# Optimization experiments

Measured on AMD Instinct MI355X. Metric: run time of the kernel, lower is better.

The kernel has to match this reference:

```python
import jax, jax.numpy as jnp
import numpy as np

BN_EPS = 1e-5


def setup_inputs() -> dict:
    key = jax.random.key(0)
    ks = jax.random.split(key, 10)
    B, C, L = 16, 512, 1024
    scale = 1.0 / np.sqrt(C)
    inp = {
        "x": jax.random.normal(ks[0], (B, C, L), dtype=jnp.float32),
        "gamma": jnp.ones((C,), jnp.float32),
        "beta": jnp.zeros((C,), jnp.float32),
        "Wq": jax.random.normal(ks[1], (C, C), jnp.float32) * scale,
        "bq": jnp.zeros((C,), jnp.float32),
        "Wk": jax.random.normal(ks[2], (C, C), jnp.float32) * scale,
        "bk": jnp.zeros((C,), jnp.float32),
        "Wv": jax.random.normal(ks[3], (C, C), jnp.float32) * scale,
        "bv": jnp.zeros((C,), jnp.float32),
        "Wp": jax.random.normal(ks[4], (C, C), jnp.float32) * scale,
        "bp": jnp.zeros((C,), jnp.float32),
    }
    return inp


def _pointwise(W, b, h):
    # Conv1d with kernel_size=1 == per-position linear: [C_out,C_in] x [B,C_in,L]
    return jnp.einsum("oc,bcl->bol", W, h) + b[None, :, None]


def reference(x, gamma, beta, Wq, bq, Wk, bk, Wv, bv, Wp, bp):
    B, C, L = x.shape
    # BatchNorm1d (training-mode batch statistics over batch & length dims)
    mean = jnp.mean(x, axis=(0, 2), keepdims=True)
    var = jnp.var(x, axis=(0, 2), keepdims=True)
    hn = (x - mean) * jax.lax.rsqrt(var + BN_EPS)
    hn = hn * gamma[None, :, None] + beta[None, :, None]

    q = _pointwise(Wq, bq, hn)  # [B,C,L]
    k = _pointwise(Wk, bk, hn)
    v = _pointwise(Wv, bv, hn)

    # attn[b,i,j] = sum_c q[b,c,i] k[b,c,j] / sqrt(C); i=query pos, j=key pos
    attn = jnp.einsum("bci,bcj->bij", q, k) * (C ** -0.5)
    attn = jax.nn.softmax(attn, axis=-1)

    # out[b,c,i] = sum_j attn[b,i,j] v[b,c,j]
    h_ = jnp.einsum("bij,bcj->bci", attn, v)
    h_ = _pointwise(Wp, bp, h_)
    return x + h_
```

## Files before the change

kernel.cpp:

```cpp
#include <hip/hip_runtime.h>
#include <hip/hip_bf16.h>


#define BB 16
#define CC 512
#define LL 1024

typedef __bf16 bf16x8 __attribute__((ext_vector_type(8)));
typedef float  f32x4  __attribute__((ext_vector_type(4)));

__device__ inline unsigned short bf16_bits(float f) {
  __hip_bfloat16 h = __float2bfloat16(f);
  return __builtin_bit_cast(unsigned short, h);
}
__device__ inline float bits_lo(unsigned int u) {
  return __builtin_bit_cast(float, u << 16);
}
__device__ inline float bits_hi(unsigned int u) {
  return __builtin_bit_cast(float, u & 0xffff0000u);
}

__global__ __launch_bounds__(256) void bn_stats(
    const float* __restrict__ x, const float* __restrict__ gamma,
    const float* __restrict__ beta, float* __restrict__ scl,
    float* __restrict__ sft) {
  int c = blockIdx.x;
  int t = threadIdx.x;
  float s = 0.f, s2 = 0.f;
  for (int b = 0; b < BB; ++b) {
    float4 v = ((const float4*)(x + ((size_t)(b * CC + c)) * LL))[t];
    s  += v.x + v.y + v.z + v.w;
    s2 += v.x * v.x + v.y * v.y + v.z * v.z + v.w * v.w;
  }
  for (int m = 32; m; m >>= 1) { s += __shfl_xor(s, m, 64); s2 += __shfl_xor(s2, m, 64); }
  __shared__ float rs[4], rs2[4];
  int wave = t >> 6, lane = t & 63;
  if (lane == 0) { rs[wave] = s; rs2[wave] = s2; }
  __syncthreads();
  if (t == 0) {
    float S  = rs[0] + rs[1] + rs[2] + rs[3];
    float S2 = rs2[0] + rs2[1] + rs2[2] + rs2[3];
    float mean = S * (1.f / 16384.f);
    float var  = S2 * (1.f / 16384.f) - mean * mean;
    float sc = gamma[c] * rsqrtf(var + 1e-5f);
    scl[c] = sc;
    sft[c] = beta[c] - mean * sc;
  }
}

__global__ __launch_bounds__(256) void cast4(
    const float* __restrict__ Wq, const float* __restrict__ Wk,
    const float* __restrict__ Wv, const float* __restrict__ Wp,
    __hip_bfloat16* __restrict__ Wqk, __hip_bfloat16* __restrict__ Wvb,
    __hip_bfloat16* __restrict__ Wpb) {
  int m = blockIdx.y;
  const float* src = m == 0 ? Wq : m == 1 ? Wk : m == 2 ? Wv : Wp;
  __hip_bfloat16* dst = m == 0 ? Wqk : m == 1 ? Wqk + 262144 : m == 2 ? Wvb : Wpb;
  int i = blockIdx.x * 256 + threadIdx.x;
  float4 v = ((const float4*)src)[i];
  ushort4 o;
  o.x = bf16_bits(v.x); o.y = bf16_bits(v.y);
  o.z = bf16_bits(v.z); o.w = bf16_bits(v.w);
  ((ushort4*)dst)[i] = o;
}

__global__ __launch_bounds__(256) void norm_t(
    const float* __restrict__ x, const float* __restrict__ scl,
    const float* __restrict__ sft, __hip_bfloat16* __restrict__ hnT) {
  __shared__ float tile[32][33];
  int l0 = blockIdx.x * 32, c0 = blockIdx.y * 32, b = blockIdx.z;
  int t = threadIdx.x;
#pragma unroll
  for (int i = 0; i < 4; ++i) {
    int idx = t + i * 256;
    int cc = idx >> 5, ll = idx & 31;
    tile[cc][ll] = x[((size_t)(b * CC + c0 + cc)) * LL + l0 + ll];
  }
  __syncthreads();
#pragma unroll
  for (int i = 0; i < 2; ++i) {
    int idx = t + i * 256;
    int ll = idx >> 4, cc = (idx & 15) * 2;
    float v0 = tile[cc][ll] * scl[c0 + cc] + sft[c0 + cc];
    float v1 = tile[cc + 1][ll] * scl[c0 + cc + 1] + sft[c0 + cc + 1];
    ushort2 o; o.x = bf16_bits(v0); o.y = bf16_bits(v1);
    *(ushort2*)(hnT + ((size_t)(b * LL + l0 + ll)) * CC + c0 + cc) = o;
  }
}

__global__ __launch_bounds__(256) void softmax_bf16(__hip_bfloat16* __restrict__ S) {
  int wave = threadIdx.x >> 6, lane = threadIdx.x & 63;
  size_t row = (size_t)blockIdx.x * 4 + wave;
  uint4* p = (uint4*)(S + row * 1024);
  uint4 r0 = p[lane * 2], r1 = p[lane * 2 + 1];
  float f[16];
  unsigned int w[8] = {r0.x, r0.y, r0.z, r0.w, r1.x, r1.y, r1.z, r1.w};
#pragma unroll
  for (int i = 0; i < 8; ++i) { f[2 * i] = bits_lo(w[i]); f[2 * i + 1] = bits_hi(w[i]); }
  float mx = f[0];
#pragma unroll
  for (int i = 1; i < 16; ++i) mx = fmaxf(mx, f[i]);
  for (int m = 32; m; m >>= 1) mx = fmaxf(mx, __shfl_xor(mx, m, 64));
  float s = 0.f;
#pragma unroll
  for (int i = 0; i < 16; ++i) { f[i] = __expf(f[i] - mx); s += f[i]; }
  for (int m = 32; m; m >>= 1) s += __shfl_xor(s, m, 64);
  float inv = 1.f / s;
  unsigned int ow[8];
#pragma unroll
  for (int i = 0; i < 8; ++i) {
    unsigned int lo = bf16_bits(f[2 * i] * inv);
    unsigned int hi = bf16_bits(f[2 * i + 1] * inv);
    ow[i] = lo | (hi << 16);
  }
  uint4 o0 = {ow[0], ow[1], ow[2], ow[3]}, o1 = {ow[4], ow[5], ow[6], ow[7]};
  p[lane * 2] = o0; p[lane * 2 + 1] = o1;
}

__device__ inline void glds(const __hip_bfloat16* g, __hip_bfloat16* l) {
  __builtin_amdgcn_global_load_lds(
      (__attribute__((address_space(1))) void*)(void*)g,
      (__attribute__((address_space(3))) void*)l, 16, 0, 0);
}

__device__ __forceinline__ void gemm_core(
    const __hip_bfloat16* __restrict__ A, int lda,
    const __hip_bfloat16* __restrict__ B, int ldb, int K,
    __hip_bfloat16* sm, f32x4 (&acc)[4][4]) {
  const int tid = threadIdx.x;
  const int wave = tid >> 6, lane = tid & 63;
  const int wm = (wave >> 1) * 64, wn = (wave & 1) * 64;
  const int row0 = tid >> 2;
  const int ke0 = (((tid & 3) ^ ((tid >> 3) & 3)) * 8);
  const int fr = lane & 15;
  const int q = lane >> 4;
  const int colA = ((q ^ ((fr >> 1) & 3)) * 8);
  const int dofs = wave * 512;

  const __hip_bfloat16* ga0 = A + (size_t)row0 * lda + ke0;
  const __hip_bfloat16* ga1 = ga0 + (size_t)64 * lda;
  const __hip_bfloat16* gb0 = B + (size_t)row0 * ldb + ke0;
  const __hip_bfloat16* gb1 = gb0 + (size_t)64 * ldb;

  __hip_bfloat16* rb = sm;
  __hip_bfloat16* nb = sm + 8192;
  __hip_bfloat16* wb = sm + 16384;

  const int niters = K >> 5;
  {
    glds(ga0, rb + dofs);          glds(ga1, rb + 2048 + dofs);
    glds(gb0, rb + 4096 + dofs);   glds(gb1, rb + 6144 + dofs);
    glds(ga0 + 32, nb + dofs);        glds(ga1 + 32, nb + 2048 + dofs);
    glds(gb0 + 32, nb + 4096 + dofs); glds(gb1 + 32, nb + 6144 + dofs);
  }
  for (int k = 0; k < niters; ++k) {
    if (k + 1 < niters) __builtin_amdgcn_s_waitcnt(0x0F74);
    else                __builtin_amdgcn_s_waitcnt(0x0F70);
    __builtin_amdgcn_s_barrier();
    if (k + 2 < niters) {
      int ko = (k + 2) * 32;
      glds(ga0 + ko, wb + dofs);          glds(ga1 + ko, wb + 2048 + dofs);
      glds(gb0 + ko, wb + 4096 + dofs);   glds(gb1 + ko, wb + 6144 + dofs);
    }
    bf16x8 af[4], bfr[4];
#pragma unroll
    for (int i = 0; i < 4; ++i) {
      af[i]  = *(const bf16x8*)(rb + (wm + i * 16 + fr) * 32 + colA);
      bfr[i] = *(const bf16x8*)(rb + 4096 + (wn + i * 16 + fr) * 32 + colA);
    }
#pragma unroll
    for (int i = 0; i < 4; ++i)
#pragma unroll
      for (int j = 0; j < 4; ++j)
        acc[i][j] = __builtin_amdgcn_mfma_f32_16x16x32_bf16(af[i], bfr[j], acc[i][j], 0, 0, 0);
    __hip_bfloat16* t = rb; rb = nb; nb = wb; wb = t;
  }
}

__global__ __launch_bounds__(256, 3) void gemm_qk(
    const __hip_bfloat16* __restrict__ Wb, const __hip_bfloat16* __restrict__ hnT,
    __hip_bfloat16* __restrict__ qT, __hip_bfloat16* __restrict__ kT,
    const float* __restrict__ bq, const float* __restrict__ bk) {
  __shared__ __align__(16) __hip_bfloat16 sm[3 * 8192];
  const int bat = blockIdx.z;
  const int m0 = blockIdx.y * 128, n0 = blockIdx.x * 128;
  f32x4 acc[4][4] = {};
  gemm_core(Wb + (size_t)m0 * 512, 512,
            hnT + (size_t)bat * LL * CC + (size_t)n0 * 512, 512, 512, sm, acc);
  const int lane = threadIdx.x & 63, wave = threadIdx.x >> 6;
  const int wm = (wave >> 1) * 64, wn = (wave & 1) * 64;
  const int crow = (lane >> 4) * 4, ccol = lane & 15;
  const int id = m0 >> 9;
  const int mloc0 = m0 & 511;
  const float* bias = id == 0 ? bq : bk;
  __hip_bfloat16* D = (id == 0 ? qT : kT) + (size_t)bat * LL * CC;
#pragma unroll
  for (int i = 0; i < 4; ++i) {
    int mg = mloc0 + wm + i * 16 + crow;
    float bv4[4];
#pragma unroll
    for (int r = 0; r < 4; ++r) bv4[r] = bias[mg + r];
#pragma unroll
    for (int j = 0; j < 4; ++j) {
      int ng = n0 + wn + j * 16 + ccol;
      ushort4 o;
      o.x = bf16_bits(acc[i][j][0] + bv4[0]);
      o.y = bf16_bits(acc[i][j][1] + bv4[1]);
      o.z = bf16_bits(acc[i][j][2] + bv4[2]);
      o.w = bf16_bits(acc[i][j][3] + bv4[3]);
      *(ushort4*)(D + (size_t)ng * 512 + mg) = o;
    }
  }
}

template <bool BIAS>
__global__ __launch_bounds__(256, 3) void gemm_bf16t(
    const __hip_bfloat16* __restrict__ A, int lda, size_t strideA,
    const __hip_bfloat16* __restrict__ B, int ldb, size_t strideB,
    __hip_bfloat16* __restrict__ D, int ldd, size_t strideD,
    const float* __restrict__ bias, float scale, int K) {
  __shared__ __align__(16) __hip_bfloat16 sm[3 * 8192];
  const int bat = blockIdx.z;
  const int m0 = blockIdx.y * 128, n0 = blockIdx.x * 128;
  f32x4 acc[4][4] = {};
  gemm_core(A + (size_t)bat * strideA + (size_t)m0 * lda, lda,
            B + (size_t)bat * strideB + (size_t)n0 * ldb, ldb, K, sm, acc);
  const int lane = threadIdx.x & 63, wave = threadIdx.x >> 6;
  const int wm = (wave >> 1) * 64, wn = (wave & 1) * 64;
  const int crow = (lane >> 4) * 4, ccol = lane & 15;
  __hip_bfloat16* Db = D + (size_t)bat * strideD;
#pragma unroll
  for (int j = 0; j < 4; ++j) {
    int ng = n0 + wn + j * 16 + ccol;
    float bn = BIAS ? bias[ng] : 0.f;
#pragma unroll
    for (int i = 0; i < 4; ++i) {
      int mg = m0 + wm + i * 16 + crow;
      ushort4 o;
      o.x = bf16_bits(acc[i][j][0] * scale + bn);
      o.y = bf16_bits(acc[i][j][1] * scale + bn);
      o.z = bf16_bits(acc[i][j][2] * scale + bn);
      o.w = bf16_bits(acc[i][j][3] * scale + bn);
      *(ushort4*)(Db + (size_t)ng * ldd + mg) = o;
    }
  }
}

__global__ __launch_bounds__(256, 3) void gemm_f32t(
    const __hip_bfloat16* __restrict__ A, int lda, size_t strideA,
    const __hip_bfloat16* __restrict__ B, int ldb,
    float* __restrict__ D, int ldd, size_t strideD,
    const float* __restrict__ bias, const float* __restrict__ resid, int K) {
  __shared__ __align__(16) __hip_bfloat16 sm[3 * 8192];
  const int bat = blockIdx.z;
  const int m0 = blockIdx.y * 128, n0 = blockIdx.x * 128;
  f32x4 acc[4][4] = {};
  gemm_core(A + (size_t)bat * strideA + (size_t)m0 * lda, lda,
            B + (size_t)n0 * ldb, ldb, K, sm, acc);
  const int lane = threadIdx.x & 63, wave = threadIdx.x >> 6;
  const int wm = (wave >> 1) * 64, wn = (wave & 1) * 64;
  const int crow = (lane >> 4) * 4, ccol = lane & 15;
  float* Db = D + (size_t)bat * strideD;
  const float* Rb = resid + (size_t)bat * strideD;
#pragma unroll
  for (int j = 0; j < 4; ++j) {
    int ng = n0 + wn + j * 16 + ccol;
    float bn = bias[ng];
#pragma unroll
    for (int i = 0; i < 4; ++i) {
      int mg = m0 + wm + i * 16 + crow;
      float4 r = *(const float4*)(Rb + (size_t)ng * ldd + mg);
      float4 o;
      o.x = acc[i][j][0] + bn + r.x;
      o.y = acc[i][j][1] + bn + r.y;
      o.z = acc[i][j][2] + bn + r.z;
      o.w = acc[i][j][3] + bn + r.w;
      *(float4*)(Db + (size_t)ng * ldd + mg) = o;
    }
  }
}

extern "C" void kernel_launch(void* const* d_in, const int* in_sizes, int n_in,
                              void* d_out, int out_size, void* d_ws, size_t ws_size,
                              hipStream_t stream) {
  const float* x     = (const float*)d_in[0];
  const float* gamma = (const float*)d_in[1];
  const float* beta  = (const float*)d_in[2];
  const float* Wq    = (const float*)d_in[3];
  const float* bq    = (const float*)d_in[4];
  const float* Wk    = (const float*)d_in[5];
  const float* bk    = (const float*)d_in[6];
  const float* Wv    = (const float*)d_in[7];
  const float* bv    = (const float*)d_in[8];
  const float* Wp    = (const float*)d_in[9];
  const float* bp    = (const float*)d_in[10];
  float* out = (float*)d_out;

  char* ws = (char*)d_ws;
  float* scl = (float*)ws;
  float* sft = scl + 512;
  __hip_bfloat16* Wqkb = (__hip_bfloat16*)(ws + 4096);
  __hip_bfloat16* Wvb  = Wqkb + 524288;
  __hip_bfloat16* Wpb  = Wvb + 262144;
  __hip_bfloat16* hnT  = Wpb + 262144;
  __hip_bfloat16* qT   = hnT + 8388608;
  __hip_bfloat16* kT   = qT + 8388608;
  __hip_bfloat16* vN   = kT + 8388608;
  __hip_bfloat16* Sb   = vN + 8388608;
  __hip_bfloat16* HT   = hnT;

  const size_t sLC = (size_t)LL * CC;
  const size_t sCL = (size_t)CC * LL;
  const size_t sLLb = (size_t)LL * LL;

  bn_stats<<<512, 256, 0, stream>>>(x, gamma, beta, scl, sft);
  cast4<<<dim3(256, 4), 256, 0, stream>>>(Wq, Wk, Wv, Wp, Wqkb, Wvb, Wpb);
  norm_t<<<dim3(32, 16, 16), 256, 0, stream>>>(x, scl, sft, hnT);

  gemm_qk<<<dim3(8, 8, 16), 256, 0, stream>>>(Wqkb, hnT, qT, kT, bq, bk);
  gemm_bf16t<true><<<dim3(4, 8, 16), 256, 0, stream>>>(
      hnT, 512, sLC, Wvb, 512, 0, vN, 1024, sCL, bv, 1.f, 512);
  gemm_bf16t<false><<<dim3(8, 8, 16), 256, 0, stream>>>(
      kT, 512, sLC, qT, 512, sLC, Sb, 1024, sLLb, nullptr,
      0.04419417382415922f, 512);
  softmax_bf16<<<4096, 256, 0, stream>>>(Sb);
  gemm_bf16t<false><<<dim3(8, 4, 16), 256, 0, stream>>>(
      vN, 1024, sCL, Sb, 1024, sLLb, HT, 512, sLC, nullptr, 1.f, 1024);
  gemm_f32t<<<dim3(4, 8, 16), 256, 0, stream>>>(
      HT, 512, sLC, Wpb, 512, out, 1024, sCL, bp, x, 512);
}
```

Before: 254.5 us.

## Fold Q/K projections into precomputed Wk^T·Wq bilinear form and simplify GEMM core

Attention scores are rewritten as hn^T (Wk^T Wq) hn plus a key-dependent bias term bq·Wk·hn. Terms that are constant along the softmax row are dropped, since softmax ignores them. A small 512x512 GEMM builds the combined matrix, a GEMV builds the per-key bias, and one fused launch produces both V and the transformed T1. This removes a full Q/K projection pass and its stored activations. Separately, the shared GEMM core drops its three-stage async LDS pipeline for a single-buffer loop with two barriers per K step, which risks exposing load latency in every GEMM. The combined matrix is also rounded to bf16, which adds precision risk.

```diff
diff --git a/kernel.cpp b/kernel.cpp
--- a/kernel.cpp
+++ b/kernel.cpp
@@ -5,6 +5,7 @@
 #define BB 16
 #define CC 512
 #define LL 1024
+#define SCALE 0.04419417382415922f
 
 typedef __bf16 bf16x8 __attribute__((ext_vector_type(8)));
 typedef float  f32x4  __attribute__((ext_vector_type(4)));
@@ -48,20 +49,52 @@
   }
 }
 
-__global__ __launch_bounds__(256) void cast4(
+__global__ __launch_bounds__(256) void cast_t(
     const float* __restrict__ Wq, const float* __restrict__ Wk,
     const float* __restrict__ Wv, const float* __restrict__ Wp,
-    __hip_bfloat16* __restrict__ Wqk, __hip_bfloat16* __restrict__ Wvb,
-    __hip_bfloat16* __restrict__ Wpb) {
+    const float* __restrict__ bq,
+    __hip_bfloat16* __restrict__ WqT, __hip_bfloat16* __restrict__ WkT,
+    __hip_bfloat16* __restrict__ Avt1, __hip_bfloat16* __restrict__ Wpb,
+    float* __restrict__ g2) {
   int m = blockIdx.y;
-  const float* src = m == 0 ? Wq : m == 1 ? Wk : m == 2 ? Wv : Wp;
-  __hip_bfloat16* dst = m == 0 ? Wqk : m == 1 ? Wqk + 262144 : m == 2 ? Wvb : Wpb;
-  int i = blockIdx.x * 256 + threadIdx.x;
-  float4 v = ((const float4*)src)[i];
-  ushort4 o;
-  o.x = bf16_bits(v.x); o.y = bf16_bits(v.y);
-  o.z = bf16_bits(v.z); o.w = bf16_bits(v.w);
-  ((ushort4*)dst)[i] = o;
+  int t = threadIdx.x;
+  if (m < 2) {
+    const float* src = m == 0 ? Wq : Wk;
+    __hip_bfloat16* dst = m == 0 ? WqT : WkT;
+    __shared__ float tile[32][33];
+    int o0 = (blockIdx.x >> 4) * 32, a0 = (blockIdx.x & 15) * 32;
+#pragma unroll
+    for (int i = 0; i < 4; ++i) {
+      int idx = t + i * 256;
+      int oo = idx >> 5, aa = idx & 31;
+      tile[oo][aa] = src[(size_t)(o0 + oo) * 512 + a0 + aa];
+    }
+    __syncthreads();
+#pragma unroll
+    for (int i = 0; i < 2; ++i) {
+      int idx = t + i * 256;
+      int aa = idx >> 4, oo = (idx & 15) * 2;
+      ushort2 o;
+      o.x = bf16_bits(tile[oo][aa]);
+      o.y = bf16_bits(tile[oo + 1][aa]);
+      *(ushort2*)(dst + (size_t)(a0 + aa) * 512 + o0 + oo) = o;
+    }
+  } else if (m < 4) {
+    const float* src = m == 2 ? Wv : Wp;
+    __hip_bfloat16* dst = m == 2 ? Avt1 : Wpb;
+    int i = blockIdx.x * 1024 + t * 4;
+    float4 v = *(const float4*)(src + i);
+    ushort4 o;
+    o.x = bf16_bits(v.x); o.y = bf16_bits(v.y);
+    o.z = bf16_bits(v.z); o.w = bf16_bits(v.w);
+    *(ushort4*)(dst + i) = o;
+  } else {
+    if (blockIdx.x >= 2) return;
+    int c = blockIdx.x * 256 + t;
+    float acc = 0.f;
+    for (int o = 0; o < 512; ++o) acc += Wk[(size_t)o * 512 + c] * bq[o];
+    g2[c] = acc;
+  }
 }
 
 __global__ __launch_bounds__(256) void norm_t(
@@ -88,15 +121,37 @@
   }
 }
 
-__global__ __launch_bounds__(256) void softmax_bf16(__hip_bfloat16* __restrict__ S) {
+__global__ __launch_bounds__(256) void w_gemv(
+    const __hip_bfloat16* __restrict__ hnT, const float* __restrict__ g2,
+    float* __restrict__ w) {
+  int wave = threadIdx.x >> 6, lane = threadIdx.x & 63;
+  size_t row = (size_t)blockIdx.x * 4 + wave;
+  bf16x8 h = *(const bf16x8*)(hnT + row * 512 + lane * 8);
+  const float* g = g2 + lane * 8;
+  float s = 0.f;
+#pragma unroll
+  for (int e = 0; e < 8; ++e) s += (float)h[e] * g[e];
+  for (int m = 32; m; m >>= 1) s += __shfl_xor(s, m, 64);
+  if (lane == 0) w[row] = s;
+}
+
+__global__ __launch_bounds__(256) void softmax_w(
+    __hip_bfloat16* __restrict__ S, const float* __restrict__ w) {
   int wave = threadIdx.x >> 6, lane = threadIdx.x & 63;
   size_t row = (size_t)blockIdx.x * 4 + wave;
   uint4* p = (uint4*)(S + row * 1024);
   uint4 r0 = p[lane * 2], r1 = p[lane * 2 + 1];
+  const float4* wp = (const float4*)(w + (row >> 10) * 1024 + lane * 16);
+  float4 w0 = wp[0], w1 = wp[1], w2 = wp[2], w3 = wp[3];
+  float wv[16] = {w0.x, w0.y, w0.z, w0.w, w1.x, w1.y, w1.z, w1.w,
+                  w2.x, w2.y, w2.z, w2.w, w3.x, w3.y, w3.z, w3.w};
   float f[16];
-  unsigned int w[8] = {r0.x, r0.y, r0.z, r0.w, r1.x, r1.y, r1.z, r1.w};
-#pragma unroll
-  for (int i = 0; i < 8; ++i) { f[2 * i] = bits_lo(w[i]); f[2 * i + 1] = bits_hi(w[i]); }
+  unsigned int ww[8] = {r0.x, r0.y, r0.z, r0.w, r1.x, r1.y, r1.z, r1.w};
+#pragma unroll
+  for (int i = 0; i < 8; ++i) {
+    f[2 * i] = bits_lo(ww[i]) + wv[2 * i];
+    f[2 * i + 1] = bits_hi(ww[i]) + wv[2 * i + 1];
+  }
   float mx = f[0];
 #pragma unroll
   for (int i = 1; i < 16; ++i) mx = fmaxf(mx, f[i]);
@@ -126,7 +181,7 @@
 __device__ __forceinline__ void gemm_core(
     const __hip_bfloat16* __restrict__ A, int lda,
     const __hip_bfloat16* __restrict__ B, int ldb, int K,
-    __hip_bfloat16* sm, f32x4 (&acc)[4][4]) {
+    __hip_bfloat16* sA, __hip_bfloat16* sB, f32x4 (&acc)[4][4]) {
   const int tid = threadIdx.x;
   const int wave = tid >> 6, lane = tid & 63;
   const int wm = (wave >> 1) * 64, wn = (wave & 1) * 64;
@@ -135,81 +190,27 @@
   const int fr = lane & 15;
   const int q = lane >> 4;
   const int colA = ((q ^ ((fr >> 1) & 3)) * 8);
-  const int dofs = wave * 512;
-
-  const __hip_bfloat16* ga0 = A + (size_t)row0 * lda + ke0;
-  const __hip_bfloat16* ga1 = ga0 + (size_t)64 * lda;
-  const __hip_bfloat16* gb0 = B + (size_t)row0 * ldb + ke0;
-  const __hip_bfloat16* gb1 = gb0 + (size_t)64 * ldb;
-
-  __hip_bfloat16* rb = sm;
-  __hip_bfloat16* nb = sm + 8192;
-  __hip_bfloat16* wb = sm + 16384;
-
-  const int niters = K >> 5;
-  {
-    glds(ga0, rb + dofs);          glds(ga1, rb + 2048 + dofs);
-    glds(gb0, rb + 4096 + dofs);   glds(gb1, rb + 6144 + dofs);
-    glds(ga0 + 32, nb + dofs);        glds(ga1 + 32, nb + 2048 + dofs);
-    glds(gb0 + 32, nb + 4096 + dofs); glds(gb1 + 32, nb + 6144 + dofs);
-  }
-  for (int k = 0; k < niters; ++k) {
-    if (k + 1 < niters) __builtin_amdgcn_s_waitcnt(0x0F74);
-    else                __builtin_amdgcn_s_waitcnt(0x0F70);
-    __builtin_amdgcn_s_barrier();
-    if (k + 2 < niters) {
-      int ko = (k + 2) * 32;
-      glds(ga0 + ko, wb + dofs);          glds(ga1 + ko, wb + 2048 + dofs);
-      glds(gb0 + ko, wb + 4096 + dofs);   glds(gb1 + ko, wb + 6144 + dofs);
-    }
+  for (int k0 = 0; k0 < K; k0 += 32) {
+    __syncthreads();
+#pragma unroll
+    for (int it = 0; it < 2; ++it) {
+      const __hip_bfloat16* ga = A + (size_t)(it * 64 + row0) * lda + (k0 + ke0);
+      const __hip_bfloat16* gb = B + (size_t)(it * 64 + row0) * ldb + (k0 + ke0);
+      glds(ga, sA + (it * 256 + wave * 64) * 8);
+      glds(gb, sB + (it * 256 + wave * 64) * 8);
+    }
+    __syncthreads();
     bf16x8 af[4], bfr[4];
 #pragma unroll
     for (int i = 0; i < 4; ++i) {
-      af[i]  = *(const bf16x8*)(rb + (wm + i * 16 + fr) * 32 + colA);
-      bfr[i] = *(const bf16x8*)(rb + 4096 + (wn + i * 16 + fr) * 32 + colA);
+      af[i]  = *(const bf16x8*)(sA + (wm + i * 16 + fr) * 32 + colA);
+      bfr[i] = *(const bf16x8*)(sB + (wn + i * 16 + fr) * 32 + colA);
     }
 #pragma unroll
     for (int i = 0; i < 4; ++i)
 #pragma unroll
       for (int j = 0; j < 4; ++j)
         acc[i][j] = __builtin_amdgcn_mfma_f32_16x16x32_bf16(af[i], bfr[j], acc[i][j], 0, 0, 0);
-    __hip_bfloat16* t = rb; rb = nb; nb = wb; wb = t;
-  }
-}
-
-__global__ __launch_bounds__(256, 3) void gemm_qk(
-    const __hip_bfloat16* __restrict__ Wb, const __hip_bfloat16* __restrict__ hnT,
-    __hip_bfloat16* __restrict__ qT, __hip_bfloat16* __restrict__ kT,
-    const float* __restrict__ bq, const float* __restrict__ bk) {
-  __shared__ __align__(16) __hip_bfloat16 sm[3 * 8192];
-  const int bat = blockIdx.z;
-  const int m0 = blockIdx.y * 128, n0 = blockIdx.x * 128;
-  f32x4 acc[4][4] = {};
-  gemm_core(Wb + (size_t)m0 * 512, 512,
-            hnT + (size_t)bat * LL * CC + (size_t)n0 * 512, 512, 512, sm, acc);
-  const int lane = threadIdx.x & 63, wave = threadIdx.x >> 6;
-  const int wm = (wave >> 1) * 64, wn = (wave & 1) * 64;
-  const int crow = (lane >> 4) * 4, ccol = lane & 15;
-  const int id = m0 >> 9;
-  const int mloc0 = m0 & 511;
-  const float* bias = id == 0 ? bq : bk;
-  __hip_bfloat16* D = (id == 0 ? qT : kT) + (size_t)bat * LL * CC;
-#pragma unroll
-  for (int i = 0; i < 4; ++i) {
-    int mg = mloc0 + wm + i * 16 + crow;
-    float bv4[4];
-#pragma unroll
-    for (int r = 0; r < 4; ++r) bv4[r] = bias[mg + r];
-#pragma unroll
-    for (int j = 0; j < 4; ++j) {
-      int ng = n0 + wn + j * 16 + ccol;
-      ushort4 o;
-      o.x = bf16_bits(acc[i][j][0] + bv4[0]);
-      o.y = bf16_bits(acc[i][j][1] + bv4[1]);
-      o.z = bf16_bits(acc[i][j][2] + bv4[2]);
-      o.w = bf16_bits(acc[i][j][3] + bv4[3]);
-      *(ushort4*)(D + (size_t)ng * 512 + mg) = o;
-    }
   }
 }
 
@@ -219,12 +220,13 @@
     const __hip_bfloat16* __restrict__ B, int ldb, size_t strideB,
     __hip_bfloat16* __restrict__ D, int ldd, size_t strideD,
     const float* __restrict__ bias, float scale, int K) {
-  __shared__ __align__(16) __hip_bfloat16 sm[3 * 8192];
+  __shared__ __align__(16) __hip_bfloat16 sA[128 * 32];
+  __shared__ __align__(16) __hip_bfloat16 sB[128 * 32];
   const int bat = blockIdx.z;
   const int m0 = blockIdx.y * 128, n0 = blockIdx.x * 128;
   f32x4 acc[4][4] = {};
   gemm_core(A + (size_t)bat * strideA + (size_t)m0 * lda, lda,
-            B + (size_t)bat * strideB + (size_t)n0 * ldb, ldb, K, sm, acc);
+            B + (size_t)bat * strideB + (size_t)n0 * ldb, ldb, K, sA, sB, acc);
   const int lane = threadIdx.x & 63, wave = threadIdx.x >> 6;
   const int wm = (wave >> 1) * 64, wn = (wave & 1) * 64;
   const int crow = (lane >> 4) * 4, ccol = lane & 15;
@@ -246,17 +248,68 @@
   }
 }
 
+__global__ __launch_bounds__(256, 3) void gemm_vt1(
+    const __hip_bfloat16* __restrict__ Ap, const __hip_bfloat16* __restrict__ hnT,
+    __hip_bfloat16* __restrict__ vN, __hip_bfloat16* __restrict__ T1T,
+    const float* __restrict__ bv) {
+  __shared__ __align__(16) __hip_bfloat16 sA[128 * 32];
+  __shared__ __align__(16) __hip_bfloat16 sB[128 * 32];
+  const int bat = blockIdx.z;
+  const int m0 = blockIdx.y * 128, n0 = blockIdx.x * 128;
+  f32x4 acc[4][4] = {};
+  gemm_core(Ap + (size_t)m0 * 512, 512,
+            hnT + (size_t)bat * LL * CC + (size_t)n0 * 512, 512, 512, sA, sB, acc);
+  const int lane = threadIdx.x & 63, wave = threadIdx.x >> 6;
+  const int wm = (wave >> 1) * 64, wn = (wave & 1) * 64;
+  const int crow = (lane >> 4) * 4, ccol = lane & 15;
+  const int mloc0 = m0 & 511;
+  if (m0 < 512) {
+    __hip_bfloat16* D = vN + (size_t)bat * CC * LL;
+#pragma unroll
+    for (int i = 0; i < 4; ++i) {
+      int mg = mloc0 + wm + i * 16 + crow;
+      float bv4[4];
+#pragma unroll
+      for (int r = 0; r < 4; ++r) bv4[r] = bv[mg + r];
+#pragma unroll
+      for (int j = 0; j < 4; ++j) {
+        int ng = n0 + wn + j * 16 + ccol;
+#pragma unroll
+        for (int r = 0; r < 4; ++r)
+          D[(size_t)(mg + r) * 1024 + ng] = __float2bfloat16(acc[i][j][r] + bv4[r]);
+      }
+    }
+  } else {
+    __hip_bfloat16* D = T1T + (size_t)bat * LL * CC;
+#pragma unroll
+    for (int j = 0; j < 4; ++j) {
+      int ng = n0 + wn + j * 16 + ccol;
+#pragma unroll
+      for (int i = 0; i < 4; ++i) {
+        int mg = mloc0 + wm + i * 16 + crow;
+        ushort4 o;
+        o.x = bf16_bits(acc[i][j][0]);
+        o.y = bf16_bits(acc[i][j][1]);
+        o.z = bf16_bits(acc[i][j][2]);
+        o.w = bf16_bits(acc[i][j][3]);
+        *(ushort4*)(D + (size_t)ng * 512 + mg) = o;
+      }
+    }
+  }
+}
+
 __global__ __launch_bounds__(256, 3) void gemm_f32t(
     const __hip_bfloat16* __restrict__ A, int lda, size_t strideA,
     const __hip_bfloat16* __restrict__ B, int ldb,
     float* __restrict__ D, int ldd, size_t strideD,
     const float* __restrict__ bias, const float* __restrict__ resid, int K) {
-  __shared__ __align__(16) __hip_bfloat16 sm[3 * 8192];
+  __shared__ __align__(16) __hip_bfloat16 sA[128 * 32];
+  __shared__ __align__(16) __hip_bfloat16 sB[128 * 32];
   const int bat = blockIdx.z;
   const int m0 = blockIdx.y * 128, n0 = blockIdx.x * 128;
   f32x4 acc[4][4] = {};
   gemm_core(A + (size_t)bat * strideA + (size_t)m0 * lda, lda,
-            B + (size_t)n0 * ldb, ldb, K, sm, acc);
+            B + (size_t)n0 * ldb, ldb, K, sA, sB, acc);
   const int lane = threadIdx.x & 63, wave = threadIdx.x >> 6;
   const int wm = (wave >> 1) * 64, wn = (wave & 1) * 64;
   const int crow = (lane >> 4) * 4, ccol = lane & 15;
@@ -295,17 +348,21 @@
   const float* Wp    = (const float*)d_in[9];
   const float* bp    = (const float*)d_in[10];
   float* out = (float*)d_out;
+  (void)bk;
 
   char* ws = (char*)d_ws;
   float* scl = (float*)ws;
   float* sft = scl + 512;
-  __hip_bfloat16* Wqkb = (__hip_bfloat16*)(ws + 4096);
-  __hip_bfloat16* Wvb  = Wqkb + 524288;
-  __hip_bfloat16* Wpb  = Wvb + 262144;
-  __hip_bfloat16* hnT  = Wpb + 262144;
-  __hip_bfloat16* qT   = hnT + 8388608;
-  __hip_bfloat16* kT   = qT + 8388608;
-  __hip_bfloat16* vN   = kT + 8388608;
+  float* g2  = sft + 512;
+  float* w   = g2 + 512;
+  __hip_bfloat16* WqT  = (__hip_bfloat16*)(w + 16384);
+  __hip_bfloat16* WkT  = WqT + 262144;
+  __hip_bfloat16* Wpb  = WkT + 262144;
+  __hip_bfloat16* Avt1 = Wpb + 262144;
+  __hip_bfloat16* Gm   = Avt1 + 262144;
+  __hip_bfloat16* hnT  = Avt1 + 524288;
+  __hip_bfloat16* T1T  = hnT + 8388608;
+  __hip_bfloat16* vN   = T1T + 8388608;
   __hip_bfloat16* Sb   = vN + 8388608;
   __hip_bfloat16* HT   = hnT;
 
@@ -314,16 +371,16 @@
   const size_t sLLb = (size_t)LL * LL;
 
   bn_stats<<<512, 256, 0, stream>>>(x, gamma, beta, scl, sft);
-  cast4<<<dim3(256, 4), 256, 0, stream>>>(Wq, Wk, Wv, Wp, Wqkb, Wvb, Wpb);
+  cast_t<<<dim3(256, 5), 256, 0, stream>>>(Wq, Wk, Wv, Wp, bq,
+                                           WqT, WkT, Avt1, Wpb, g2);
   norm_t<<<dim3(32, 16, 16), 256, 0, stream>>>(x, scl, sft, hnT);
-
-  gemm_qk<<<dim3(8, 8, 16), 256, 0, stream>>>(Wqkb, hnT, qT, kT, bq, bk);
-  gemm_bf16t<true><<<dim3(4, 8, 16), 256, 0, stream>>>(
-      hnT, 512, sLC, Wvb, 512, 0, vN, 1024, sCL, bv, 1.f, 512);
+  gemm_bf16t<false><<<dim3(4, 4, 1), 256, 0, stream>>>(
+      WkT, 512, 0, WqT, 512, 0, Gm, 512, 0, nullptr, SCALE, 512);
+  w_gemv<<<4096, 256, 0, stream>>>(hnT, g2, w);
+  gemm_vt1<<<dim3(8, 8, 16), 256, 0, stream>>>(Avt1, hnT, vN, T1T, bv);
   gemm_bf16t<false><<<dim3(8, 8, 16), 256, 0, stream>>>(
-      kT, 512, sLC, qT, 512, sLC, Sb, 1024, sLLb, nullptr,
-      0.04419417382415922f, 512);
-  softmax_bf16<<<4096, 256, 0, stream>>>(Sb);
+      T1T, 512, sLC, hnT, 512, sLC, Sb, 1024, sLLb, nullptr, 1.f, 512);
+  softmax_w<<<4096, 256, 0, stream>>>(Sb, w);
   gemm_bf16t<false><<<dim3(8, 4, 16), 256, 0, stream>>>(
       vN, 1024, sCL, Sb, 1024, sLLb, HT, 512, sLC, nullptr, 1.f, 1024);
   gemm_f32t<<<dim3(4, 8, 16), 256, 0, stream>>>(
```

Result: slower. 273.9 us (+7.6%).
